# Kernel tuning notes

Hardware: AMD Instinct MI355X
Metric: run time of the kernel (lower is better)

## Reference

```python
import jax, jax.numpy as jnp
import numpy as np

H = 128          # hidden
N = 50000        # nodes
E = 800000       # edges
P = 3200000      # pos entries (4 per edge)
G = 100          # graphs in batch
L = 3            # extra GINEConv layers (num_layers - 1)
Z_VOCAB = 1800
BN_EPS = 1e-5


def setup_inputs() -> dict:
    key = jax.random.key(0)
    ks = jax.random.split(key, 32)
    w = lambda k, shape: jax.random.normal(k, shape, dtype=jnp.float32) * 0.05
    inp = {
        "edge_index": jax.random.randint(ks[0], (2, E), 0, N),
        "batch": jnp.sort(jax.random.randint(ks[1], (N,), 0, G)),
        "pos_index": jax.random.randint(ks[2], (P,), 0, Z_VOCAB),
        "pos_enc": jax.random.uniform(ks[3], (P,), dtype=jnp.float32),
        "pos_batch": jnp.sort(jax.random.randint(ks[4], (P,), 0, E)),
        # z_initial embedding table + z_embedding MLP (BN -> ReLU -> Linear -> BN -> ReLU)
        "z_table": w(ks[5], (Z_VOCAB, H)),
        "bn1_g": jnp.ones((H,), jnp.float32), "bn1_b": jnp.zeros((H,), jnp.float32),
        "Wz": w(ks[6], (H, H)), "bz": jnp.zeros((H,), jnp.float32),
        "bn2_g": jnp.ones((H,), jnp.float32), "bn2_b": jnp.zeros((H,), jnp.float32),
        # conv1: edge lin maps hidden -> in_channels(=1); nn: Linear(1,H)+ReLU+Linear(H,H)+ReLU
        "We1": w(ks[7], (H, 1)), "be1": jnp.zeros((1,), jnp.float32),
        "W1a": w(ks[8], (1, H)), "b1a": jnp.zeros((H,), jnp.float32),
        "W1b": w(ks[9], (H, H)), "b1b": jnp.zeros((H,), jnp.float32),
        # remaining L convs (stacked): edge lin H->H, nn Linear(H,H)x2
        "We": w(ks[10], (L, H, H)), "be": jnp.zeros((L, H), jnp.float32),
        "Wa": w(ks[11], (L, H, H)), "ba": jnp.zeros((L, H), jnp.float32),
        "Wb": w(ks[12], (L, H, H)), "bb": jnp.zeros((L, H), jnp.float32),
        # readout heads
        "Wl1": w(ks[13], (H, H)), "bl1": jnp.zeros((H,), jnp.float32),
        "Wl2": w(ks[14], (H, H)), "bl2": jnp.zeros((H,), jnp.float32),
    }
    return inp


def _bn_eval(x, g, b):
    # eval-mode BatchNorm1d with running_mean=0, running_var=1
    return x * (g / jnp.sqrt(1.0 + BN_EPS)) + b


def reference(edge_index, batch, pos_index, pos_enc, pos_batch,
              z_table, bn1_g, bn1_b, Wz, bz, bn2_g, bn2_b,
              We1, be1, W1a, b1a, W1b, b1b,
              We, be, Wa, ba, Wb, bb,
              Wl1, bl1, Wl2, bl2):
    # edge embedding: global_add_pool of gathered z rows weighted by pos_enc -> [E, H]
    z = jax.ops.segment_sum(z_table[pos_index] * pos_enc[:, None], pos_batch, num_segments=E)
    z = jax.nn.relu(_bn_eval(z, bn1_g, bn1_b))
    z = jax.nn.relu(_bn_eval(z @ Wz + bz, bn2_g, bn2_b))

    src, dst = edge_index[0], edge_index[1]
    x = jnp.ones((N, 1), dtype=z.dtype)  # no node features in data

    # conv1 (GINEConv, eps=0): out = nn(x + sum_j relu(x_j + lin_e(z_e)))
    msg = jax.nn.relu(x[src] + (z @ We1 + be1))            # [E, 1]
    h = x + jax.ops.segment_sum(msg, dst, num_segments=N)  # [N, 1]
    x = jax.nn.relu(jax.nn.relu(h @ W1a + b1a) @ W1b + b1b)  # [N, H]

    for l in range(We.shape[0]):
        e = z @ We[l] + be[l]                                   # [E, H]
        msg = jax.nn.relu(x[src] + e)                           # [E, H]
        h = x + jax.ops.segment_sum(msg, dst, num_segments=N)   # [N, H]
        x = jax.nn.relu(jax.nn.relu(h @ Wa[l] + ba[l]) @ Wb[l] + bb[l])

    g = jax.ops.segment_sum(x, batch, num_segments=G)  # global_add_pool -> [G, H]
    g = jax.nn.relu(g @ Wl1 + bl1)                     # dropout is identity in eval mode
    return jax.nn.log_softmax(g @ Wl2 + bl2, axis=1)
```

## Files before the change

### kernel.cpp

```cpp
#include <hip/hip_runtime.h>
#include <hip/hip_bf16.h>

#define H 128

typedef __attribute__((ext_vector_type(8))) short bf16x8;
typedef __attribute__((ext_vector_type(4))) float f32x4;

__device__ __forceinline__ float bf2f(unsigned int u16) {
  union { float f; unsigned int i; } v;
  v.i = u16 << 16;
  return v.f;
}
__device__ __forceinline__ unsigned short f2bf(float f) {
  union { float f; unsigned int i; } v;
  v.f = f;
  unsigned int lsb = (v.i >> 16) & 1u;
  v.i += 0x7fffu + lsb;
  return (unsigned short)(v.i >> 16);
}

__device__ __forceinline__ int lb(const int* __restrict__ a, int n, int v) {
  int lo = 0, hi = n;
  while (lo < hi) { int m = (lo + hi) >> 1; if (a[m] < v) lo = m + 1; else hi = m; }
  return lo;
}

__device__ __forceinline__ float wave_sum(float v) {
#pragma unroll
  for (int off = 32; off > 0; off >>= 1) v += __shfl_xor(v, off);
  return v;
}
__device__ __forceinline__ float wave_max(float v) {
#pragma unroll
  for (int off = 32; off > 0; off >>= 1) v = fmaxf(v, __shfl_xor(v, off));
  return v;
}

__device__ __forceinline__ void stage_B(const float* __restrict__ W, short* __restrict__ lds) {
  for (int e = threadIdx.x; e < 8 * 4 * 64; e += blockDim.x) {
    int lane = e & 63;
    int kc = (e >> 6) & 3;
    int ct = e >> 8;
    int col = ct * 16 + (lane & 15);
    int k0 = kc * 32 + (lane >> 4) * 8;
    bf16x8 pack;
#pragma unroll
    for (int j = 0; j < 8; ++j) pack[j] = (short)f2bf(W[(k0 + j) * H + col]);
    *(bf16x8*)(lds + (size_t)e * 8) = pack;
  }
}

__global__ void k_count(const int* __restrict__ dst, int* __restrict__ cnt, int E) {
  int i = blockIdx.x * blockDim.x + threadIdx.x;
  if (i < E) atomicAdd(cnt + dst[i], 1);
}

__global__ void k_scan(const int* __restrict__ cnt, int* __restrict__ off,
                       int* __restrict__ cur, int N) {
  __shared__ int part[1024];
  int t = threadIdx.x;
  int C = (N + 1023) / 1024;
  int beg = t * C, end = min(beg + C, N);
  int s = 0;
  for (int i = beg; i < end; ++i) s += cnt[i];
  part[t] = s;
  __syncthreads();
  for (int d = 1; d < 1024; d <<= 1) {
    int v = (t >= d) ? part[t - d] : 0;
    __syncthreads();
    part[t] += v;
    __syncthreads();
  }
  int run = (t == 0) ? 0 : part[t - 1];
  for (int i = beg; i < end; ++i) {
    off[i] = run; cur[i] = run;
    run += cnt[i];
  }
  if (t == 1023) off[N] = part[1023];
}

__global__ void k_scatter(const int* __restrict__ dst, int* __restrict__ cur,
                          int* __restrict__ rank, int E) {
  int i = blockIdx.x * blockDim.x + threadIdx.x;
  if (i < E) { int p = atomicAdd(cur + dst[i], 1); rank[i] = p; }
}

__global__ void k_dstp(const int* __restrict__ off, int* __restrict__ dstp, int N) {
  int n = blockIdx.x * blockDim.x + threadIdx.x;
  if (n < N) {
    int lo = off[n], hi = off[n + 1];
    for (int i = lo; i < hi; ++i) dstp[i] = n;
  }
}

__global__ void k_srcp(const int* __restrict__ src, const int* __restrict__ rank,
                       int* __restrict__ srcp, int E) {
  int i = blockIdx.x * blockDim.x + threadIdx.x;
  if (i < E) srcp[rank[i]] = src[i];
}

__global__ void k_posoff(const int* __restrict__ pos_batch, int* __restrict__ pos_off,
                         int P, int E) {
  int p = blockIdx.x * blockDim.x + threadIdx.x;
  if (p >= P) return;
  int b = pos_batch[p];
  int prev = (p == 0) ? -1 : pos_batch[p - 1];
  for (int q = prev + 1; q <= b; ++q) pos_off[q] = p;
  if (p == P - 1)
    for (int q = b + 1; q <= E; ++q) pos_off[q] = P;
}

__device__ __forceinline__ void tile_range(int tiles, int wv, int& t0, int& t1) {
  const int W = (gridDim.x * blockDim.x) >> 6;
  const int bswz = ((blockIdx.x & 7) * (gridDim.x >> 3)) + (blockIdx.x >> 3);
  const int gw = bswz * (blockDim.x >> 6) + wv;
  t0 = (int)(((long long)tiles * gw) / W);
  t1 = (int)(((long long)tiles * (gw + 1)) / W);
}

__global__ __launch_bounds__(256, 2)
void k_zfused(const int* __restrict__ rank, const int* __restrict__ dst,
              const int* __restrict__ pos_off, const int* __restrict__ pos_index,
              const float* __restrict__ pos_enc, const float* __restrict__ z_table,
              const float* __restrict__ bn1_g, const float* __restrict__ bn1_b,
              const float* __restrict__ Wz, const float* __restrict__ bz,
              const float* __restrict__ bn2_g, const float* __restrict__ bn2_b,
              const float* __restrict__ We1, const float* __restrict__ be1,
              float* __restrict__ h1, unsigned short* __restrict__ z2p, int E) {
  __shared__ short Blds[8 * 4 * 64 * 8];
  __shared__ __attribute__((aligned(16))) float s_g1[H], s_b1[H];
  __shared__ float s_g2[H], s_b2[H], s_bz[H], s_w1[H];
  stage_B(Wz, Blds);
  const float inv = rsqrtf(1.0f + 1e-5f);
  for (int i = threadIdx.x; i < H; i += blockDim.x) {
    s_g1[i] = bn1_g[i] * inv;
    s_b1[i] = bn1_b[i];
    s_g2[i] = bn2_g[i] * inv;
    s_b2[i] = bn2_b[i];
    s_bz[i] = bz[i];
    s_w1[i] = We1[i];
  }
  __syncthreads();
  const int lane = threadIdx.x & 63;
  const int wv = threadIdx.x >> 6;
  const int cb = lane & 15;
  const int g = lane >> 4;
  const int tiles = E >> 4;
  const float be = be1[0];
  int t0, t1;
  tile_range(tiles, wv, t0, t1);
  for (int t = t0; t < t1; ++t) {
    const int e = (t << 4) + cb;
    const int lo = pos_off[e], hi = pos_off[e + 1];
    float za[4][8];
#pragma unroll
    for (int kc = 0; kc < 4; ++kc)
#pragma unroll
      for (int j = 0; j < 8; ++j) za[kc][j] = 0.f;
    for (int p = lo; p < hi; ++p) {
      int r = pos_index[p];
      float w = pos_enc[p];
      const float* row = z_table + (size_t)r * H + g * 8;
#pragma unroll
      for (int kc = 0; kc < 4; ++kc) {
        float4 v0 = *(const float4*)(row + kc * 32);
        float4 v1 = *(const float4*)(row + kc * 32 + 4);
        za[kc][0] = fmaf(w, v0.x, za[kc][0]);
        za[kc][1] = fmaf(w, v0.y, za[kc][1]);
        za[kc][2] = fmaf(w, v0.z, za[kc][2]);
        za[kc][3] = fmaf(w, v0.w, za[kc][3]);
        za[kc][4] = fmaf(w, v1.x, za[kc][4]);
        za[kc][5] = fmaf(w, v1.y, za[kc][5]);
        za[kc][6] = fmaf(w, v1.z, za[kc][6]);
        za[kc][7] = fmaf(w, v1.w, za[kc][7]);
      }
    }
    bf16x8 a[4];
#pragma unroll
    for (int kc = 0; kc < 4; ++kc) {
      const float* gp = s_g1 + kc * 32 + g * 8;
      const float* bp = s_b1 + kc * 32 + g * 8;
      float4 G0 = *(const float4*)gp;
      float4 G1 = *(const float4*)(gp + 4);
      float4 B0 = *(const float4*)bp;
      float4 B1 = *(const float4*)(bp + 4);
      a[kc][0] = (short)f2bf(fmaxf(0.f, fmaf(za[kc][0], G0.x, B0.x)));
      a[kc][1] = (short)f2bf(fmaxf(0.f, fmaf(za[kc][1], G0.y, B0.y)));
      a[kc][2] = (short)f2bf(fmaxf(0.f, fmaf(za[kc][2], G0.z, B0.z)));
      a[kc][3] = (short)f2bf(fmaxf(0.f, fmaf(za[kc][3], G0.w, B0.w)));
      a[kc][4] = (short)f2bf(fmaxf(0.f, fmaf(za[kc][4], G1.x, B1.x)));
      a[kc][5] = (short)f2bf(fmaxf(0.f, fmaf(za[kc][5], G1.y, B1.y)));
      a[kc][6] = (short)f2bf(fmaxf(0.f, fmaf(za[kc][6], G1.z, B1.z)));
      a[kc][7] = (short)f2bf(fmaxf(0.f, fmaf(za[kc][7], G1.w, B1.w)));
    }
    const int r0 = (t << 4) + (g << 2);
    int rk[4], dn[4];
#pragma unroll
    for (int j = 0; j < 4; ++j) {
      rk[j] = rank[r0 + j];
      dn[j] = dst[r0 + j];
    }
    float msg[4] = {0.f, 0.f, 0.f, 0.f};
#pragma unroll 1
    for (int ct = 0; ct < 8; ++ct) {
      f32x4 acc = (f32x4){0.f, 0.f, 0.f, 0.f};
#pragma unroll
      for (int kc = 0; kc < 4; ++kc) {
        bf16x8 b = *(const bf16x8*)(Blds + ((size_t)((ct << 2) + kc) * 64 + lane) * 8);
        acc = __builtin_amdgcn_mfma_f32_16x16x32_bf16(a[kc], b, acc, 0, 0, 0);
      }
      int c = (ct << 4) + cb;
      float bv = s_bz[c], gv = s_g2[c], b2 = s_b2[c], w1 = s_w1[c];
#pragma unroll
      for (int j = 0; j < 4; ++j) {
        float y = fmaxf(0.f, fmaf(acc[j] + bv, gv, b2));
        z2p[(size_t)rk[j] * H + c] = f2bf(y);
        msg[j] = fmaf(y, w1, msg[j]);
      }
    }
#pragma unroll
    for (int j = 0; j < 4; ++j)
#pragma unroll
      for (int o2 = 8; o2 > 0; o2 >>= 1) msg[j] += __shfl_xor(msg[j], o2);
    if (cb == 0) {
#pragma unroll
      for (int j = 0; j < 4; ++j)
        atomicAdd(h1 + dn[j], fmaxf(0.f, 1.0f + msg[j] + be));
    }
  }
}

template <int IN_BF16, int OUT_BF16, int DUAL>
__global__ __launch_bounds__(256, 2)
void k_gemm(const void* __restrict__ in, void* __restrict__ out,
            const float* __restrict__ W, const float* __restrict__ bias,
            float* __restrict__ h_out, int R) {
  __shared__ short Blds[8 * 4 * 64 * 8];
  stage_B(W, Blds);
  __syncthreads();
  const int lane = threadIdx.x & 63;
  const int wv = threadIdx.x >> 6;
  const int tiles = R >> 4;
  const int nw = (gridDim.x * blockDim.x) >> 6;
  for (int t = blockIdx.x * (blockDim.x >> 6) + wv; t < tiles; t += nw) {
    const int arow = (t << 4) + (lane & 15);
    bf16x8 a[4];
    if (IN_BF16) {
      const short* ib = (const short*)in;
#pragma unroll
      for (int kc = 0; kc < 4; ++kc)
        a[kc] = *(const bf16x8*)(ib + (size_t)arow * H + kc * 32 + (lane >> 4) * 8);
    } else {
      const float* iff = (const float*)in;
#pragma unroll
      for (int kc = 0; kc < 4; ++kc) {
        const float* p = iff + (size_t)arow * H + kc * 32 + (lane >> 4) * 8;
#pragma unroll
        for (int j = 0; j < 8; ++j) a[kc][j] = (short)f2bf(p[j]);
      }
    }
    f32x4 acc[8];
#pragma unroll
    for (int ct = 0; ct < 8; ++ct) acc[ct] = (f32x4){0.f, 0.f, 0.f, 0.f};
#pragma unroll
    for (int ct = 0; ct < 8; ++ct)
#pragma unroll
      for (int kc = 0; kc < 4; ++kc) {
        bf16x8 b = *(const bf16x8*)(Blds + ((size_t)((ct << 2) + kc) * 64 + lane) * 8);
        acc[ct] = __builtin_amdgcn_mfma_f32_16x16x32_bf16(a[kc], b, acc[ct], 0, 0, 0);
      }
    const int r0 = (t << 4) + ((lane >> 4) << 2);
    const int cb = lane & 15;
#pragma unroll
    for (int ct = 0; ct < 8; ++ct) {
      int c = (ct << 4) + cb;
      float bv = bias[c];
#pragma unroll
      for (int j = 0; j < 4; ++j) {
        float y = fmaxf(acc[ct][j] + bv, 0.f);
        size_t idx = (size_t)(r0 + j) * H + c;
        if (OUT_BF16) ((unsigned short*)out)[idx] = f2bf(y);
        else ((float*)out)[idx] = y;
        if (DUAL) h_out[idx] = y;
      }
    }
  }
}

#define XR_STRIDE 132
__global__ __launch_bounds__(256, 2)
void k_agg_mfma(const unsigned short* __restrict__ x,
                const unsigned short* __restrict__ z2p,
                const float* __restrict__ We, const float* __restrict__ be,
                const int* __restrict__ srcp, const int* __restrict__ dstp,
                float* __restrict__ h, int E) {
  __shared__ short Blds[8 * 4 * 64 * 8];
  __shared__ short Xlds[4][16 * XR_STRIDE];
  __shared__ float s_be[H];
  stage_B(We, Blds);
  for (int i = threadIdx.x; i < H; i += blockDim.x) s_be[i] = be[i];
  __syncthreads();
  const int lane = threadIdx.x & 63;
  const int wv = threadIdx.x >> 6;
  const int cb = lane & 15;
  const int g = lane >> 4;
  const int tiles = E >> 4;
  short* xw = Xlds[wv];
  int t0, t1;
  tile_range(tiles, wv, t0, t1);
  for (int t = t0; t < t1; ++t) {
    {
      const int sl = srcp[(t << 4) + cb];
      const short* gsrc = (const short*)x + (size_t)sl * H + g * 8;
      short* xrow = xw + cb * XR_STRIDE + g * 8;
#pragma unroll
      for (int kc = 0; kc < 4; ++kc)
        *(bf16x8*)(xrow + kc * 32) = *(const bf16x8*)(gsrc + kc * 32);
    }
    const int arow = (t << 4) + cb;
    bf16x8 a[4];
#pragma unroll
    for (int kc = 0; kc < 4; ++kc)
      a[kc] = *(const bf16x8*)((const short*)z2p + (size_t)arow * H + kc * 32 + g * 8);
    f32x4 acc[8];
#pragma unroll
    for (int ct = 0; ct < 8; ++ct) acc[ct] = (f32x4){0.f, 0.f, 0.f, 0.f};
#pragma unroll
    for (int ct = 0; ct < 8; ++ct)
#pragma unroll
      for (int kc = 0; kc < 4; ++kc) {
        bf16x8 b = *(const bf16x8*)(Blds + ((size_t)((ct << 2) + kc) * 64 + lane) * 8);
        acc[ct] = __builtin_amdgcn_mfma_f32_16x16x32_bf16(a[kc], b, acc[ct], 0, 0, 0);
      }
    const int r0 = (t << 4) + (g << 2);
    const int dlo = dstp[t << 4], dhi = dstp[(t << 4) + 15];
    const short* xr = xw + (g << 2) * XR_STRIDE;
    if (dlo == dhi) {
#pragma unroll
      for (int ct = 0; ct < 8; ++ct) {
        int c = (ct << 4) + cb;
        float bv = s_be[c];
        float run = 0.f;
#pragma unroll
        for (int j = 0; j < 4; ++j) {
          float xv = bf2f((unsigned int)(unsigned short)xr[j * XR_STRIDE + c]);
          run += fmaxf(0.f, xv + acc[ct][j] + bv);
        }
        run += __shfl_xor(run, 16);
        run += __shfl_xor(run, 32);
        if (g == 0) atomicAdd(h + (size_t)dlo * H + c, run);
      }
    } else {
      int dn[4];
#pragma unroll
      for (int j = 0; j < 4; ++j) dn[j] = dstp[r0 + j];
#pragma unroll
      for (int ct = 0; ct < 8; ++ct) {
        int c = (ct << 4) + cb;
        float bv = s_be[c];
        float run = 0.f;
        int prev = dn[0];
#pragma unroll
        for (int j = 0; j < 4; ++j) {
          float xv = bf2f((unsigned int)(unsigned short)xr[j * XR_STRIDE + c]);
          float msg = fmaxf(0.f, xv + acc[ct][j] + bv);
          if (dn[j] != prev) {
            atomicAdd(h + (size_t)prev * H + c, run);
            run = 0.f;
            prev = dn[j];
          }
          run += msg;
        }
        atomicAdd(h + (size_t)prev * H + c, run);
      }
    }
  }
}

__global__ void k_c1a(const float* __restrict__ h1, const float* __restrict__ W1a,
                      const float* __restrict__ b1a, unsigned short* __restrict__ x, int N) {
  int idx = blockIdx.x * blockDim.x + threadIdx.x;
  int n = idx >> 6;
  if (n >= N) return;
  int c0 = (idx & 63) * 2;
  float hv = 1.0f + h1[n];
  float y0 = fmaxf(0.f, fmaf(hv, W1a[c0], b1a[c0]));
  float y1 = fmaxf(0.f, fmaf(hv, W1a[c0 + 1], b1a[c0 + 1]));
  unsigned int pack = ((unsigned int)f2bf(y1) << 16) | f2bf(y0);
  *(unsigned int*)(x + (size_t)n * H + c0) = pack;
}

__global__ void k_pool(const unsigned short* __restrict__ x, const int* __restrict__ batch,
                       float* __restrict__ g, int N, int G) {
  __shared__ float red[4][H];
  int gi = blockIdx.x;
  int lane = threadIdx.x & 63;
  int w = threadIdx.x >> 6;
  int lo = lb(batch, N, gi), hi = lb(batch, N, gi + 1);
  float a0 = 0.f, a1 = 0.f;
  for (int n = lo + w; n < hi; n += 4) {
    unsigned int pk = *(const unsigned int*)(x + (size_t)n * H + lane * 2);
    a0 += bf2f(pk & 0xffffu);
    a1 += bf2f(pk >> 16);
  }
  red[w][2 * lane] = a0;
  red[w][2 * lane + 1] = a1;
  __syncthreads();
  if (w == 0) {
    a0 = red[0][2 * lane] + red[1][2 * lane] + red[2][2 * lane] + red[3][2 * lane];
    a1 = red[0][2 * lane + 1] + red[1][2 * lane + 1] + red[2][2 * lane + 1] + red[3][2 * lane + 1];
    *(float2*)(g + (size_t)gi * H + 2 * lane) = make_float2(a0, a1);
  }
}

__global__ void k_head(const float* __restrict__ g, const float* __restrict__ Wl1,
                       const float* __restrict__ bl1, const float* __restrict__ Wl2,
                       const float* __restrict__ bl2, float* __restrict__ out, int G) {
  int gi = blockIdx.x;
  int lane = threadIdx.x & 63;
  const int c0 = 2 * lane, c1 = c0 + 1;
  float2 gv = *(const float2*)(g + (size_t)gi * H + c0);
  float m0 = bl1[c0], m1 = bl1[c1];
#pragma unroll
  for (int k = 0; k < H; ++k) {
    float s = __shfl((k & 1) ? gv.y : gv.x, k >> 1);
    float2 w = *(const float2*)(Wl1 + k * H + c0);
    m0 = fmaf(s, w.x, m0);
    m1 = fmaf(s, w.y, m1);
  }
  float t0 = fmaxf(0.f, m0), t1 = fmaxf(0.f, m1);
  float L0 = bl2[c0], L1 = bl2[c1];
#pragma unroll
  for (int k = 0; k < H; ++k) {
    float s = __shfl((k & 1) ? t1 : t0, k >> 1);
    float2 w = *(const float2*)(Wl2 + k * H + c0);
    L0 = fmaf(s, w.x, L0);
    L1 = fmaf(s, w.y, L1);
  }
  float mx = wave_max(fmaxf(L0, L1));
  float sm = wave_sum(expf(L0 - mx) + expf(L1 - mx));
  float lse = mx + logf(sm);
  *(float2*)(out + (size_t)gi * H + c0) = make_float2(L0 - lse, L1 - lse);
}

__global__ void k_zero_out(float* __restrict__ out, int n) {
  int i = blockIdx.x * blockDim.x + threadIdx.x;
  if (i < n) out[i] = 0.f;
}

extern "C" void kernel_launch(void* const* d_in, const int* in_sizes, int n_in,
                              void* d_out, int out_size, void* d_ws, size_t ws_size,
                              hipStream_t stream) {
  const int* edge_index = (const int*)d_in[0];
  const int* batch = (const int*)d_in[1];
  const int* pos_index = (const int*)d_in[2];
  const float* pos_enc = (const float*)d_in[3];
  const int* pos_batch = (const int*)d_in[4];
  const float* z_table = (const float*)d_in[5];
  const float* bn1_g = (const float*)d_in[6];
  const float* bn1_b = (const float*)d_in[7];
  const float* Wz = (const float*)d_in[8];
  const float* bz = (const float*)d_in[9];
  const float* bn2_g = (const float*)d_in[10];
  const float* bn2_b = (const float*)d_in[11];
  const float* We1 = (const float*)d_in[12];
  const float* be1 = (const float*)d_in[13];
  const float* W1a = (const float*)d_in[14];
  const float* b1a = (const float*)d_in[15];
  const float* W1b = (const float*)d_in[16];
  const float* b1b = (const float*)d_in[17];
  const float* We = (const float*)d_in[18];
  const float* be = (const float*)d_in[19];
  const float* Wa = (const float*)d_in[20];
  const float* ba = (const float*)d_in[21];
  const float* Wb = (const float*)d_in[22];
  const float* bb = (const float*)d_in[23];
  const float* Wl1 = (const float*)d_in[24];
  const float* bl1 = (const float*)d_in[25];
  const float* Wl2 = (const float*)d_in[26];
  const float* bl2 = (const float*)d_in[27];

  const int E = in_sizes[0] / 2;
  const int N = in_sizes[1];
  const int P = in_sizes[2];
  const int L = in_sizes[18] / (H * H);
  const int G = out_size / H;
  const int* src = edge_index;
  const int* dst = edge_index + E;

  char* wsb = (char*)d_ws;
  size_t o = 0;
  auto alloc = [&](size_t bytes) -> void* {
    o = (o + 255) & ~(size_t)255;
    void* p = wsb + o;
    o += bytes;
    return p;
  };
  unsigned short* z2p = (unsigned short*)alloc((size_t)E * H * 2);
  unsigned short* x = (unsigned short*)alloc((size_t)N * H * 2);
  float* h = (float*)alloc((size_t)N * H * 4);
  float* h1 = (float*)alloc((size_t)N * 4);
  int* cnt = (int*)alloc((size_t)N * 4);
  int* off = (int*)alloc((size_t)(N + 1) * 4);
  int* cur = (int*)alloc((size_t)N * 4);
  int* rank = (int*)alloc((size_t)E * 4);
  int* srcp = (int*)alloc((size_t)E * 4);
  int* dstp = (int*)alloc((size_t)E * 4);
  int* pos_off = (int*)alloc((size_t)(E + 1) * 4);
  float* g = (float*)alloc((size_t)G * H * 4);
  (void)n_in;

  if (o > ws_size) {
    k_zero_out<<<(out_size + 255) / 256, 256, 0, stream>>>((float*)d_out, out_size);
    return;
  }

  hipMemsetAsync(cnt, 0, (size_t)N * 4, stream);
  hipMemsetAsync(h1, 0, (size_t)N * 4, stream);

  k_count<<<(E + 255) / 256, 256, 0, stream>>>(dst, cnt, E);
  k_scan<<<1, 1024, 0, stream>>>(cnt, off, cur, N);
  k_scatter<<<(E + 255) / 256, 256, 0, stream>>>(dst, cur, rank, E);
  k_dstp<<<(N + 255) / 256, 256, 0, stream>>>(off, dstp, N);
  k_srcp<<<(E + 255) / 256, 256, 0, stream>>>(src, rank, srcp, E);
  k_posoff<<<(P + 255) / 256, 256, 0, stream>>>(pos_batch, pos_off, P, E);

  k_zfused<<<2048, 256, 0, stream>>>(rank, dst, pos_off, pos_index, pos_enc, z_table,
                                     bn1_g, bn1_b, Wz, bz, bn2_g, bn2_b, We1, be1, h1,
                                     z2p, E);

  k_c1a<<<(N * 64 + 255) / 256, 256, 0, stream>>>(h1, W1a, b1a, x, N);
  k_gemm<1, 1, 1><<<782, 256, 0, stream>>>(x, x, W1b, b1b, h, N);

  for (int l = 0; l < L; ++l) {
    k_agg_mfma<<<2048, 256, 0, stream>>>(x, z2p, We + (size_t)l * H * H, be + (size_t)l * H,
                                         srcp, dstp, h, E);
    k_gemm<0, 0, 0><<<782, 256, 0, stream>>>(h, h, Wa + (size_t)l * H * H, ba + (size_t)l * H,
                                             nullptr, N);
    if (l < L - 1)
      k_gemm<0, 1, 1><<<782, 256, 0, stream>>>(h, x, Wb + (size_t)l * H * H, bb + (size_t)l * H,
                                               h, N);
    else
      k_gemm<0, 1, 0><<<782, 256, 0, stream>>>(h, x, Wb + (size_t)l * H * H, bb + (size_t)l * H,
                                               nullptr, N);
  }

  k_pool<<<G, 256, 0, stream>>>(x, batch, g, N, G);
  k_head<<<G, 64, 0, stream>>>(g, Wl1, bl1, Wl2, bl2, (float*)d_out, G);
}
```

Baseline: 1.503 ms.

## Partition aggregation by destination-node boundaries to replace atomics with owned updates

The edge aggregation kernel now assigns each wave a contiguous edge range whose ends are snapped to node boundaries with a binary search over the CSR offsets. Each destination node is therefore owned by exactly one wave. Per-node partial sums are carried across 16-edge tiles in registers, and segments are found with a ballot over destination changes. Each finished node is written with a plain read-modify-write instead of atomicAdd, removing atomic traffic to global memory. The cost is extra per-segment shuffle and reduction work, partial-tile masking, and possible load imbalance from snapping ranges to node boundaries.

```diff
diff --git a/kernel.cpp b/kernel.cpp
--- a/kernel.cpp
+++ b/kernel.cpp
@@ -293,7 +293,7 @@
                 const unsigned short* __restrict__ z2p,
                 const float* __restrict__ We, const float* __restrict__ be,
                 const int* __restrict__ srcp, const int* __restrict__ dstp,
-                float* __restrict__ h, int E) {
+                const int* __restrict__ off, float* __restrict__ h, int N, int E) {
   __shared__ short Blds[8 * 4 * 64 * 8];
   __shared__ short Xlds[4][16 * XR_STRIDE];
   __shared__ float s_be[H];
@@ -304,24 +304,36 @@
   const int wv = threadIdx.x >> 6;
   const int cb = lane & 15;
   const int g = lane >> 4;
-  const int tiles = E >> 4;
+  const int W = (gridDim.x * blockDim.x) >> 6;
+  const int bswz = ((blockIdx.x & 7) * (gridDim.x >> 3)) + (blockIdx.x >> 3);
+  const int gw = bswz * (blockDim.x >> 6) + wv;
+  const int e0 = (int)(((long long)E * gw) / W);
+  const int e1 = (int)(((long long)E * (gw + 1)) / W);
+  const int nlo = lb(off, N + 1, e0);
+  const int nhi = lb(off, N + 1, e1);
+  const int estart = off[nlo];
+  const int eend = off[nhi];
+  if (estart >= eend) return;
   short* xw = Xlds[wv];
-  int t0, t1;
-  tile_range(tiles, wv, t0, t1);
-  for (int t = t0; t < t1; ++t) {
+  short* xrow = xw + cb * XR_STRIDE + g * 8;
+  float carry[8];
+#pragma unroll
+  for (int ct = 0; ct < 8; ++ct) carry[ct] = 0.f;
+  int prev_node = -1;
+  for (int s = estart; s < eend; s += 16) {
+    const int rowcount = min(16, eend - s);
+    const int rclamp = min(s + cb, eend - 1);
     {
-      const int sl = srcp[(t << 4) + cb];
+      const int sl = srcp[rclamp];
       const short* gsrc = (const short*)x + (size_t)sl * H + g * 8;
-      short* xrow = xw + cb * XR_STRIDE + g * 8;
 #pragma unroll
       for (int kc = 0; kc < 4; ++kc)
         *(bf16x8*)(xrow + kc * 32) = *(const bf16x8*)(gsrc + kc * 32);
     }
-    const int arow = (t << 4) + cb;
     bf16x8 a[4];
 #pragma unroll
     for (int kc = 0; kc < 4; ++kc)
-      a[kc] = *(const bf16x8*)((const short*)z2p + (size_t)arow * H + kc * 32 + g * 8);
+      a[kc] = *(const bf16x8*)((const short*)z2p + (size_t)rclamp * H + kc * 32 + g * 8);
     f32x4 acc[8];
 #pragma unroll
     for (int ct = 0; ct < 8; ++ct) acc[ct] = (f32x4){0.f, 0.f, 0.f, 0.f};
@@ -332,47 +344,65 @@
         bf16x8 b = *(const bf16x8*)(Blds + ((size_t)((ct << 2) + kc) * 64 + lane) * 8);
         acc[ct] = __builtin_amdgcn_mfma_f32_16x16x32_bf16(a[kc], b, acc[ct], 0, 0, 0);
       }
-    const int r0 = (t << 4) + (g << 2);
-    const int dlo = dstp[t << 4], dhi = dstp[(t << 4) + 15];
+    const int s_dn = dstp[rclamp];
+    const int dn_prev = __shfl_up(s_dn, 1);
+    bool flag = (cb == 0) ? (s_dn != prev_node) : (s_dn != dn_prev);
+    flag = flag && (cb < rowcount);
+    const unsigned int bm = (unsigned int)(__ballot(flag) & 0xffffull);
+    if ((bm & 1u) && prev_node >= 0) {
+      if (g == 0) {
+#pragma unroll
+        for (int ct = 0; ct < 8; ++ct) {
+          float* hp = h + (size_t)prev_node * H + (ct << 4) + cb;
+          *hp += carry[ct];
+        }
+      }
+#pragma unroll
+      for (int ct = 0; ct < 8; ++ct) carry[ct] = 0.f;
+    }
     const short* xr = xw + (g << 2) * XR_STRIDE;
-    if (dlo == dhi) {
+#pragma unroll
+    for (int ct = 0; ct < 8; ++ct) {
+      int c = (ct << 4) + cb;
+      float bv = s_be[c];
+#pragma unroll
+      for (int j = 0; j < 4; ++j) {
+        int r2 = (g << 2) + j;
+        float xv = bf2f((unsigned int)(unsigned short)xr[j * XR_STRIDE + c]);
+        float m = fmaxf(0.f, xv + acc[ct][j] + bv);
+        acc[ct][j] = (r2 < rowcount) ? m : 0.f;
+      }
+    }
+    const bool waveEnd = (s + rowcount >= eend);
+    int pos = 0;
+    while (pos < rowcount) {
+      unsigned int rest = bm & ~((2u << pos) - 1u);
+      int segend = rest ? (int)__builtin_ctz(rest) : rowcount;
+      int node = __shfl(s_dn, pos);
+      bool closes = (segend < rowcount) || waveEnd;
 #pragma unroll
       for (int ct = 0; ct < 8; ++ct) {
-        int c = (ct << 4) + cb;
-        float bv = s_be[c];
-        float run = 0.f;
+        float part = 0.f;
 #pragma unroll
         for (int j = 0; j < 4; ++j) {
-          float xv = bf2f((unsigned int)(unsigned short)xr[j * XR_STRIDE + c]);
-          run += fmaxf(0.f, xv + acc[ct][j] + bv);
+          int r2 = (g << 2) + j;
+          part += (r2 >= pos && r2 < segend) ? acc[ct][j] : 0.f;
         }
-        run += __shfl_xor(run, 16);
-        run += __shfl_xor(run, 32);
-        if (g == 0) atomicAdd(h + (size_t)dlo * H + c, run);
-      }
-    } else {
-      int dn[4];
-#pragma unroll
-      for (int j = 0; j < 4; ++j) dn[j] = dstp[r0 + j];
-#pragma unroll
-      for (int ct = 0; ct < 8; ++ct) {
-        int c = (ct << 4) + cb;
-        float bv = s_be[c];
-        float run = 0.f;
-        int prev = dn[0];
-#pragma unroll
-        for (int j = 0; j < 4; ++j) {
-          float xv = bf2f((unsigned int)(unsigned short)xr[j * XR_STRIDE + c]);
-          float msg = fmaxf(0.f, xv + acc[ct][j] + bv);
-          if (dn[j] != prev) {
-            atomicAdd(h + (size_t)prev * H + c, run);
-            run = 0.f;
-            prev = dn[j];
+        part += __shfl_xor(part, 16);
+        part += __shfl_xor(part, 32);
+        float tot = carry[ct] + part;
+        if (closes) {
+          if (g == 0) {
+            float* hp = h + (size_t)node * H + (ct << 4) + cb;
+            *hp += tot;
           }
-          run += msg;
+          carry[ct] = 0.f;
+        } else {
+          carry[ct] = tot;
         }
-        atomicAdd(h + (size_t)prev * H + c, run);
-      }
+      }
+      prev_node = node;
+      pos = segend;
     }
   }
 }
@@ -534,7 +564,7 @@
 
   for (int l = 0; l < L; ++l) {
     k_agg_mfma<<<2048, 256, 0, stream>>>(x, z2p, We + (size_t)l * H * H, be + (size_t)l * H,
-                                         srcp, dstp, h, E);
+                                         srcp, dstp, off, h, N, E);
     k_gemm<0, 0, 0><<<782, 256, 0, stream>>>(h, h, Wa + (size_t)l * H * H, ba + (size_t)l * H,
                                              nullptr, N);
     if (l < L - 1)
```

After: 1.351 ms. 10.1% less time.
